# Optimization experiments

Hardware: AMD Instinct MI355X
Metric: run time of the kernel (lower is better)

The kernel has to match this reference:

```python
import jax, jax.numpy as jnp
import numpy as np
from jax.ops import segment_sum, segment_max

N, E, B = 100000, 400000, 2048
F_NODE, F_EDGE, G_DIM = 7, 3, 10
HID, H, C, L, T = 128, 4, 32, 4, 5
EPS = 1e-5
NEG_SLOPE = 0.2

def setup_inputs():
    key = jax.random.key(0)
    ks = iter(jax.random.split(key, 64))
    def nrm(shape, fan_in):
        return jax.random.normal(next(ks), shape, jnp.float32) / np.float32(np.sqrt(fan_in))
    return {
        "x": jax.random.normal(next(ks), (N, F_NODE), jnp.float32),
        "edge_index": jax.random.randint(next(ks), (2, E), 0, N),
        "edge_attr": jax.random.normal(next(ks), (E, F_EDGE), jnp.float32),
        "batch": jnp.sort(jax.random.randint(next(ks), (N,), 0, B)),
        "global_features": jax.random.normal(next(ks), (B, G_DIM), jnp.float32),
        "node_w": nrm((F_NODE, HID), F_NODE), "node_b": jnp.zeros((HID,), jnp.float32),
        "edge_w": nrm((F_EDGE, HID), F_EDGE), "edge_b": jnp.zeros((HID,), jnp.float32),
        "gat_lin_w": nrm((L, HID, H * C), HID),
        "gat_edge_w": nrm((L, HID, H * C), HID),
        "att_src": nrm((L, H, C), C), "att_dst": nrm((L, H, C), C), "att_edge": nrm((L, H, C), C),
        "gat_bias": jnp.zeros((L, H * C), jnp.float32),
        "bn_gamma": jnp.ones((L, HID), jnp.float32), "bn_beta": jnp.zeros((L, HID), jnp.float32),
        "bn_mean": jnp.zeros((L, HID), jnp.float32), "bn_var": jnp.ones((L, HID), jnp.float32),
        "gc_w": nrm((3 * HID, HID), 3 * HID), "gc_b": jnp.zeros((HID,), jnp.float32),
        "gf1_w": nrm((G_DIM, HID // 2), G_DIM), "gf1_b": jnp.zeros((HID // 2,), jnp.float32),
        "gf2_w": nrm((HID // 2, HID // 2), HID // 2), "gf2_b": jnp.zeros((HID // 2,), jnp.float32),
        "p1_w": nrm((HID + HID // 2, HID), HID + HID // 2), "p1_b": jnp.zeros((HID,), jnp.float32),
        "p2_w": nrm((HID, HID // 2), HID), "p2_b": jnp.zeros((HID // 2,), jnp.float32),
        "p3_w": nrm((HID // 2, T), HID // 2), "p3_b": jnp.zeros((T,), jnp.float32),
    }

def _forward(x, edge_attr, global_features,
             node_w, node_b, edge_w, edge_b,
             gat_lin_w, gat_edge_w, att_src, att_dst, att_edge, gat_bias,
             bn_gamma, bn_beta, bn_mean, bn_var,
             gc_w, gc_b, gf1_w, gf1_b, gf2_w, gf2_b,
             p1_w, p1_b, p2_w, p2_b, p3_w, p3_b,
             edge_index, batch):
    n = x.shape[0]
    b = global_features.shape[0]
    src, dst = edge_index[0], edge_index[1]
    loop = jnp.arange(n)

    h = x @ node_w + node_b                       # [N, HID]
    e = edge_attr @ edge_w + edge_b               # [E, HID]

    # PyG add_self_loops with fill_value='mean': self-loop edge feature is the
    # mean of incoming edge features (0 for isolated nodes).
    deg = segment_sum(jnp.ones((src.shape[0],), h.dtype), dst, num_segments=n)
    e_loop = segment_sum(e, dst, num_segments=n) / jnp.maximum(deg, 1.0)[:, None]
    fsrc = jnp.concatenate([src, loop])
    fdst = jnp.concatenate([dst, loop])
    fe = jnp.concatenate([e, e_loop], axis=0)     # [E+N, HID]

    for i in range(L):
        h_res = h
        xh = (h @ gat_lin_w[i]).reshape(n, H, C)
        eh = (fe @ gat_edge_w[i]).reshape(-1, H, C)
        a_s = jnp.einsum('nhc,hc->nh', xh, att_src[i])
        a_d = jnp.einsum('nhc,hc->nh', xh, att_dst[i])
        a_e = jnp.einsum('ehc,hc->eh', eh, att_edge[i])
        alpha = jax.nn.leaky_relu(a_s[fsrc] + a_d[fdst] + a_e, NEG_SLOPE)  # [E+N, H]
        # segment softmax over destination neighborhoods (self loops => nonempty)
        amax = segment_max(alpha, fdst, num_segments=n)
        expa = jnp.exp(alpha - amax[fdst])
        denom = segment_sum(expa, fdst, num_segments=n)
        coef = expa / denom[fdst]
        out = segment_sum(xh[fsrc] * coef[..., None], fdst, num_segments=n)
        out = out.reshape(n, H * C) + gat_bias[i]
        # BatchNorm (eval-mode running stats)
        out = (out - bn_mean[i]) * (bn_gamma[i] / jnp.sqrt(bn_var[i] + EPS)) + bn_beta[i]
        h = jax.nn.relu(out) + h_res

    # multi-pool readout
    cnt = segment_sum(jnp.ones((n,), h.dtype), batch, num_segments=b)
    gsum = segment_sum(h, batch, num_segments=b)
    gmean = gsum / jnp.maximum(cnt, 1.0)[:, None]
    gmax = segment_max(h, batch, num_segments=b)
    gmax = jnp.where(cnt[:, None] > 0, gmax, 0.0)
    graph = jnp.concatenate([gmean, gmax, gsum], axis=1)   # [B, 3*HID]
    graph = jax.nn.relu(graph @ gc_w + gc_b)
    glob = jax.nn.relu(global_features @ gf1_w + gf1_b) @ gf2_w + gf2_b
    comb = jnp.concatenate([graph, glob], axis=1)          # [B, HID + HID//2]
    hid = jax.nn.relu(comb @ p1_w + p1_b)
    hid = jax.nn.relu(hid @ p2_w + p2_b)
    return hid @ p3_w + p3_b                               # [B, T]

def reference(x, edge_index, edge_attr, batch, global_features,
              node_w, node_b, edge_w, edge_b,
              gat_lin_w, gat_edge_w, att_src, att_dst, att_edge, gat_bias,
              bn_gamma, bn_beta, bn_mean, bn_var,
              gc_w, gc_b, gf1_w, gf1_b, gf2_w, gf2_b,
              p1_w, p1_b, p2_w, p2_b, p3_w, p3_b):
    return _forward(x, edge_attr, global_features,
                    node_w, node_b, edge_w, edge_b,
                    gat_lin_w, gat_edge_w, att_src, att_dst, att_edge, gat_bias,
                    bn_gamma, bn_beta, bn_mean, bn_var,
                    gc_w, gc_b, gf1_w, gf1_b, gf2_w, gf2_b,
                    p1_w, p1_b, p2_w, p2_b, p3_w, p3_b,
                    edge_index, batch)
```

## Files before the change

### kernel.cpp

```cpp
#include <hip/hip_runtime.h>

#define N_NODES 100000
#define N_EDGES 400000
#define N_GRAPHS 2048
#define HID 128
#define NLAYER 4
#define TOUT 5
#define EPSV 1e-5f
#define SLOPE 0.2f
#define MAXDEG 32
#define NB 98
#define GEMM_BLOCKS 782

typedef float v4f __attribute__((ext_vector_type(4)));
typedef __bf16 v8bf __attribute__((ext_vector_type(8)));

static __device__ __forceinline__ unsigned short f2bf_bits(float f){
  unsigned u = __builtin_bit_cast(unsigned, f);
  unsigned r = u + 0x7fffu + ((u >> 16) & 1u);
  return (unsigned short)(r >> 16);
}
static __device__ __forceinline__ float bfbits2f(unsigned short s){
  unsigned u = ((unsigned)s) << 16;
  return __builtin_bit_cast(float, u);
}
static __device__ __forceinline__ float bflo(unsigned u){
  return __builtin_bit_cast(float, u << 16);
}
static __device__ __forceinline__ float bfhi(unsigned u){
  return __builtin_bit_cast(float, u & 0xffff0000u);
}
static __device__ __forceinline__ float lrelu(float v){
  return v>0.f ? v : SLOPE*v;
}


__global__ void k_setup(const float* __restrict__ gat_edge_w, const float* __restrict__ att_edge,
                        const float* __restrict__ edge_w, const float* __restrict__ edge_b,
                        const float* __restrict__ gat_bias, const float* __restrict__ gamma,
                        const float* __restrict__ beta, const float* __restrict__ mean,
                        const float* __restrict__ var, const float* __restrict__ gat_lin_w,
                        const float* __restrict__ att_src, const float* __restrict__ att_dst,
                        const float* __restrict__ x, const float* __restrict__ nw,
                        const float* __restrict__ nb, unsigned* __restrict__ h16,
                        float* __restrict__ mebuf, float* __restrict__ bnA, float* __restrict__ bnS,
                        unsigned short* __restrict__ whiE, unsigned short* __restrict__ wloE,
                        unsigned short* __restrict__ whi,
                        int* __restrict__ deg, int* __restrict__ fill){
  int bid = blockIdx.x, t = threadIdx.x;
  if(bid < 16){
    int wv = t>>6, lane = t&63;
    int o = bid*4 + wv;
    int li = (o<48)? (o&15) : (o-48);
    int f = o>>4;
    int l = li>>2, hh = li&3;
    int c = lane&31, kk = lane>>5;
    float at_c = att_edge[l*128 + hh*32 + c];
    float acc = 0.f;
    #pragma unroll 8
    for(int t2=0; t2<64; ++t2){
      int k = kk*64 + t2;
      float wk = (o<48)? edge_w[f*128+k] : edge_b[k];
      acc += wk * gat_edge_w[l*16384 + k*128 + hh*32 + c];
    }
    acc *= at_c;
    acc += __shfl_xor(acc,1); acc += __shfl_xor(acc,2); acc += __shfl_xor(acc,4);
    acc += __shfl_xor(acc,8); acc += __shfl_xor(acc,16); acc += __shfl_xor(acc,32);
    if(lane==0) mebuf[o] = acc;
  } else if(bid == 16){
    for(int i=t; i<NLAYER*HID; i+=256){
      int l_ = i>>7, pos = i&127, lane = pos>>2, j = pos&3;
      int ch = ((lane>>3)<<5) + ((lane&7)<<1) + ((j&1)<<4) + (j>>1);
      int src = l_*128 + ch;
      float A = gamma[src]*rsqrtf(var[src]+EPSV);
      bnA[i] = A;
      bnS[i] = (gat_bias[src]-mean[src])*A + beta[src];
    }
  } else if(bid <= 1040){
    int wave = t>>6, lane = t&63;
    int i = (bid-17)*8 + wave*2 + (lane>>5);
    int l_ = i>>11, rest = i&2047, kp = rest>>4, col = rest&15;
    int sub = lane&31;
    float val = 0.f;
    if(col < 8){
      int h_ = col&3, isdst = col>>2;
      int ch = ((kp>>5)<<5) + ((kp&1)<<4) + ((kp&31)>>1);
      const float* at = (isdst? att_dst : att_src);
      val = gat_lin_w[l_*16384 + ch*128 + h_*32 + sub] * at[l_*128 + h_*32 + sub];
    }
    val += __shfl_xor(val,1); val += __shfl_xor(val,2); val += __shfl_xor(val,4);
    val += __shfl_xor(val,8); val += __shfl_xor(val,16);
    if(sub == 0){
      unsigned short hi = f2bf_bits(val);
      unsigned short lo = f2bf_bits(val - bfbits2f(hi));
      int kb=kp>>5, quad=(kp>>3)&3, jj=kp&7, lane2=quad*16+col;
      int dst = ((l_*4+kb)*64 + lane2)*8 + jj;
      whiE[dst]=hi; wloE[dst]=lo;
    }
  } else if(bid <= 1296){
    int tg = (bid-1041)*256 + t;
    int base = tg>>9, off = tg&511;
    int l = base>>5, kb=(base>>3)&3, cg=base&7;
    int lane = off>>3, j = off&7;
    int quad = lane>>4, r = lane&15;
    int kp = kb*32 + quad*8 + j;
    int k = ((kp>>5)<<5) | ((kp&1)<<4) | ((kp&31)>>1);
    whi[tg] = f2bf_bits(gat_lin_w[l*16384 + k*128 + cg*16 + r]);
  } else if(bid <= 1687){
    int tg = (bid-1297)*256 + t;
    if(tg < N_NODES){ deg[tg]=0; fill[tg]=0; }
  } else {
    int node = (bid-1688)*4 + (t>>6);
    int c = t&63;
    int ch = ((c>>4)<<5) + (c&15);
    float a0 = nb[ch], a1 = nb[ch+16];
    #pragma unroll
    for(int f=0; f<7; ++f){
      float xv = x[node*7+f];
      a0 += xv*nw[f*HID+ch];
      a1 += xv*nw[f*HID+ch+16];
    }
    unsigned p = (unsigned)f2bf_bits(a0) | ((unsigned)f2bf_bits(a1)<<16);
    h16[(size_t)node*64 + c] = p;
  }
}

__global__ void k_deg(const int* __restrict__ ei, int* __restrict__ deg){
  int e = blockIdx.x*256 + threadIdx.x;
  if(e < N_EDGES) atomicAdd(&deg[ei[N_EDGES+e]], 1);
}

__global__ void k_scan1(const int* __restrict__ deg, int* __restrict__ part){
  __shared__ int s[256];
  int t=threadIdx.x; int base = blockIdx.x*1024 + t*4;
  int sum=0;
  #pragma unroll
  for(int j=0;j<4;++j){ int i=base+j; sum += (i<N_NODES)? deg[i]:0; }
  s[t]=sum; __syncthreads();
  for(int off=128; off>0; off>>=1){ if(t<off) s[t]+=s[t+off]; __syncthreads(); }
  if(t==0) part[blockIdx.x]=s[0];
}
__global__ void k_scan3(const int* __restrict__ deg, const int* __restrict__ part,
                        int* __restrict__ rowptr){
  __shared__ int s[256];
  int t=threadIdx.x, b=blockIdx.x;
  int g = 0, tot = 0;
  for(int i=0;i<NB;++i){ int v = part[i]; g += (i<b)? v : 0; tot += v; }
  if(b==0 && t==0) rowptr[N_NODES]=tot;
  int base = b*1024 + t*4;
  int v[4]; int sum=0; int pre[4];
  #pragma unroll
  for(int j=0;j<4;++j){ int i=base+j; v[j]=(i<N_NODES)?deg[i]:0; pre[j]=sum; sum+=v[j]; }
  s[t]=sum; __syncthreads();
  for(int off=1; off<256; off<<=1){
    int xv = (t>=off)? s[t-off]:0; __syncthreads();
    s[t]+=xv; __syncthreads();
  }
  int toff = (t>0)? s[t-1]:0;
  #pragma unroll
  for(int j=0;j<4;++j){ int i=base+j; if(i<N_NODES) rowptr[i]=g+toff+pre[j]; }
}

__global__ void k_gemm(const unsigned short* __restrict__ h16,
                       const unsigned short* __restrict__ whi,
                       const unsigned short* __restrict__ whiE,
                       const unsigned short* __restrict__ wloE,
                       unsigned* __restrict__ xhb, float* __restrict__ as_, float* __restrict__ ad_,
                       const int* __restrict__ ei, const float* __restrict__ ea,
                       const int* __restrict__ rowptr, int* __restrict__ fill,
                       int* __restrict__ csr_src, float* __restrict__ ea_csr){
  if(blockIdx.x >= GEMM_BLOCKS){
    int e = (blockIdx.x - GEMM_BLOCKS)*256 + threadIdx.x;
    if(e < N_EDGES){
      int dst = ei[N_EDGES+e];
      int pos = rowptr[dst] + atomicAdd(&fill[dst],1);
      csr_src[pos] = ei[e];
      v4f q = {ea[e*3], ea[e*3+1], ea[e*3+2], 0.f};
      ((v4f*)ea_csr)[pos] = q;
    }
    return;
  }
  __shared__ unsigned sxh[4][2][16*68];
  int wave = threadIdx.x>>6, lane = threadIdx.x&63;
  int base = blockIdx.x*128;
  int q = lane>>4, r = lane&15;
  int r0[2];
  r0[0] = base + wave*16;
  r0[1] = base + 64 + wave*16;
  if(r0[0] > N_NODES-16) r0[0] = N_NODES-16;
  if(r0[1] > N_NODES-16) r0[1] = N_NODES-16;
  v8bf av[2][4];
  #pragma unroll
  for(int tt=0;tt<2;++tt){
    const unsigned short* hrow = h16 + (size_t)(r0[tt] + r)*HID;
    #pragma unroll
    for(int kb=0;kb<4;++kb)
      av[tt][kb] = *(const v8bf*)(hrow + kb*32 + q*8);
  }
  v4f acc[2][8];
  #pragma unroll
  for(int cg=0;cg<8;++cg){
    v4f a0 = {0.f,0.f,0.f,0.f}, a1 = {0.f,0.f,0.f,0.f};
    #pragma unroll
    for(int kb=0;kb<4;++kb){
      v8bf bhi = *(const v8bf*)(whi + ((kb*8+cg)*64 + lane)*8);
      a0 = __builtin_amdgcn_mfma_f32_16x16x32_bf16(av[0][kb], bhi, a0, 0,0,0);
      a1 = __builtin_amdgcn_mfma_f32_16x16x32_bf16(av[1][kb], bhi, a1, 0,0,0);
    }
    acc[0][cg]=a0; acc[1][cg]=a1;
  }
  v4f acc8[2] = {{0.f,0.f,0.f,0.f},{0.f,0.f,0.f,0.f}};
  #pragma unroll
  for(int kb=0;kb<4;++kb){
    v8bf bhi = *(const v8bf*)(whiE + (kb*64 + lane)*8);
    v8bf blo = *(const v8bf*)(wloE + (kb*64 + lane)*8);
    #pragma unroll
    for(int tt=0;tt<2;++tt){
      acc8[tt] = __builtin_amdgcn_mfma_f32_16x16x32_bf16(av[tt][kb], blo, acc8[tt], 0,0,0);
      acc8[tt] = __builtin_amdgcn_mfma_f32_16x16x32_bf16(av[tt][kb], bhi, acc8[tt], 0,0,0);
    }
  }
  #pragma unroll
  for(int tt=0;tt<2;++tt){
    #pragma unroll
    for(int m=0;m<4;++m){
      #pragma unroll
      for(int reg=0;reg<4;++reg){
        unsigned pack = (unsigned)f2bf_bits(acc[tt][2*m][reg]) | ((unsigned)f2bf_bits(acc[tt][2*m+1][reg])<<16);
        sxh[wave][tt][(q*4+reg)*68 + m*16 + r] = pack;
      }
    }
  }
  __syncthreads();
  {
    int rr = lane>>4, c4 = lane&15;
    #pragma unroll
    for(int tt=0;tt<2;++tt){
      #pragma unroll
      for(int rg=0; rg<4; ++rg){
        int i = rg*4 + rr;
        uint4 v = *(const uint4*)&sxh[wave][tt][i*68 + c4*4];
        *(uint4*)(xhb + (size_t)(r0[tt] + i)*64 + c4*4) = v;
      }
    }
  }
  #pragma unroll
  for(int tt=0;tt<2;++tt){
    if(r < 4){
      #pragma unroll
      for(int reg=0;reg<4;++reg)
        as_[(size_t)(r0[tt] + q*4 + reg)*4 + r] = acc8[tt][reg];
    } else if(r < 8){
      #pragma unroll
      for(int reg=0;reg<4;++reg)
        ad_[(size_t)(r0[tt] + q*4 + reg)*4 + (r-4)] = acc8[tt][reg];
    }
  }
}

__global__ void k_aggr(const unsigned* __restrict__ xhb, const float* __restrict__ as_,
    const float* __restrict__ ad_, const float* __restrict__ ea_csr,
    const float* __restrict__ mebuf,
    const int* __restrict__ rowptr, const int* __restrict__ csr_src,
    const float* __restrict__ bnA_l, const float* __restrict__ bnS_l,
    unsigned* __restrict__ h16, int layer){
  __shared__ float lds_coef[4][MAXDEG*4];
  __shared__ int   lds_src[4][MAXDEG];
  int w = threadIdx.x>>6, lane = threadIdx.x&63;
  int node = blockIdx.x*4 + w;
  if(node >= N_NODES) return;
  int s = rowptr[node], e = rowptr[node+1];
  int deg = e - s;
  int l = lane&31, half = lane>>5, hh2 = l>>3;
  const uint2* xrow = (const uint2*)xhb;
  float a0,a1,a2,a3;

  if(deg <= MAXDEG){
    int eidx = lane>>2, h = lane&3;
    int li = layer*4+h;
    float mec0=mebuf[li], mec1=mebuf[16+li], mec2=mebuf[32+li], meb=mebuf[48+li];
    float ad_h = ad_[node*4+h];
    int j0 = eidx;
    float t0 = 0.f, g0 = 0.f;
    int s0 = node;
    bool v0 = (j0 < deg);
    if(v0){
      s0 = csr_src[s+j0];
      v4f qq = ((const v4f*)ea_csr)[s+j0];
      t0 = qq.x*mec0 + qq.y*mec1 + qq.z*mec2;
      g0 = lrelu(as_[s0*4+h] + ad_h + t0 + meb);
    }
    float ts, ds, inv;
    if(deg <= 16){
      ts = t0;
      ts += __shfl_xor(ts,4); ts += __shfl_xor(ts,8);
      ts += __shfl_xor(ts,16); ts += __shfl_xor(ts,32);
      float lt = (deg>0) ? ts/(float)deg + meb : 0.f;
      float al = lrelu(as_[node*4+h] + ad_h + lt);
      float e0 = v0 ? __expf(g0-al) : 0.f;
      ds = e0;
      ds += __shfl_xor(ds,4); ds += __shfl_xor(ds,8);
      ds += __shfl_xor(ds,16); ds += __shfl_xor(ds,32);
      inv = 1.f/(ds+1.f);
      lds_src[w][j0] = s0;
      lds_coef[w][j0*4+h] = e0*inv;
    } else {
      int j1 = 16+eidx;
      float t1 = 0.f, g1 = 0.f;
      int s1 = node;
      bool v1 = (j1 < deg);
      if(v1){
        s1 = csr_src[s+j1];
        v4f qq = ((const v4f*)ea_csr)[s+j1];
        t1 = qq.x*mec0 + qq.y*mec1 + qq.z*mec2;
        g1 = lrelu(as_[s1*4+h] + ad_h + t1 + meb);
      }
      ts = t0+t1;
      ts += __shfl_xor(ts,4); ts += __shfl_xor(ts,8);
      ts += __shfl_xor(ts,16); ts += __shfl_xor(ts,32);
      float lt = ts/(float)deg + meb;
      float al = lrelu(as_[node*4+h] + ad_h + lt);
      float e0 = v0 ? __expf(g0-al) : 0.f;
      float e1 = v1 ? __expf(g1-al) : 0.f;
      ds = e0+e1;
      ds += __shfl_xor(ds,4); ds += __shfl_xor(ds,8);
      ds += __shfl_xor(ds,16); ds += __shfl_xor(ds,32);
      inv = 1.f/(ds+1.f);
      if(h==0){ lds_src[w][j0]=s0; lds_src[w][j1]=s1; }
      lds_coef[w][j0*4+h] = e0*inv;
      lds_coef[w][j1*4+h] = e1*inv;
    }
    float cs4 = __shfl(inv, hh2);
    uint2 su = xrow[(size_t)node*32 + l];
    int pdeg = (deg+3)&~3;
    a0=a1=a2=a3=0.f;
    for(int j=0;j<pdeg;j+=4){
      float ca = lds_coef[w][(j+half)*4+hh2];
      float cb = lds_coef[w][(j+2+half)*4+hh2];
      int sa = lds_src[w][j+half], sb = lds_src[w][j+2+half];
      uint2 ua = xrow[(size_t)sa*32+l];
      uint2 ub = xrow[(size_t)sb*32+l];
      a0 += ca*bflo(ua.x) + cb*bflo(ub.x);
      a1 += ca*bfhi(ua.x) + cb*bfhi(ub.x);
      a2 += ca*bflo(ua.y) + cb*bflo(ub.y);
      a3 += ca*bfhi(ua.y) + cb*bfhi(ub.y);
    }
    a0 += __shfl_xor(a0,32); a1 += __shfl_xor(a1,32);
    a2 += __shfl_xor(a2,32); a3 += __shfl_xor(a3,32);
    a0 += cs4*bflo(su.x); a1 += cs4*bfhi(su.x);
    a2 += cs4*bflo(su.y); a3 += cs4*bfhi(su.y);
  } else {
    int li = layer*4+hh2;
    float mec0=mebuf[li], mec1=mebuf[16+li], mec2=mebuf[32+li], meb=mebuf[48+li];
    float adv = ad_[node*4+hh2];
    float ts = 0.f;
    for(int j=s;j<e;++j){
      v4f qq = ((const v4f*)ea_csr)[j];
      ts += qq.x*mec0 + qq.y*mec1 + qq.z*mec2;
    }
    float al = lrelu(as_[node*4+hh2] + adv + ts/(float)deg + meb);
    float m = al, d = 1.f;
    uint2 su = xrow[(size_t)node*32 + l];
    float c0=bflo(su.x),c1=bfhi(su.x),c2=bflo(su.y),c3=bfhi(su.y);
    for(int j=s;j<e;++j){
      int sr = csr_src[j];
      v4f qq = ((const v4f*)ea_csr)[j];
      float b = lrelu(as_[sr*4+hh2] + adv + qq.x*mec0+qq.y*mec1+qq.z*mec2+meb);
      uint2 uv = xrow[(size_t)sr*32 + l];
      float nm = fmaxf(m,b);
      float sc = __expf(m-nm), eb = __expf(b-nm);
      d = d*sc + eb;
      c0 = c0*sc + eb*bflo(uv.x); c1 = c1*sc + eb*bfhi(uv.x);
      c2 = c2*sc + eb*bflo(uv.y); c3 = c3*sc + eb*bfhi(uv.y);
      m = nm;
    }
    float inv2 = 1.f/d;
    a0=c0*inv2; a1=c1*inv2; a2=c2*inv2; a3=c3*inv2;
  }

  if(half==0){
    const v4f* A4 = (const v4f*)bnA_l;
    const v4f* S4 = (const v4f*)bnS_l;
    v4f A = A4[l], S = S4[l];
    uint2 hr = ((const uint2*)h16)[(size_t)node*32 + l];
    float o0 = fmaxf(a0*A.x+S.x, 0.f) + bflo(hr.x);
    float o1 = fmaxf(a1*A.y+S.y, 0.f) + bfhi(hr.x);
    float o2 = fmaxf(a2*A.z+S.z, 0.f) + bflo(hr.y);
    float o3 = fmaxf(a3*A.w+S.w, 0.f) + bfhi(hr.y);
    uint2 p;
    p.x = (unsigned)f2bf_bits(o0) | ((unsigned)f2bf_bits(o1)<<16);
    p.y = (unsigned)f2bf_bits(o2) | ((unsigned)f2bf_bits(o3)<<16);
    ((uint2*)h16)[(size_t)node*32 + l] = p;
  }
}

__global__ void k_tail(const unsigned* __restrict__ h16, const int* __restrict__ batch,
   const float* __restrict__ gf,
   const float* __restrict__ gc_w, const float* __restrict__ gc_b,
   const float* __restrict__ gf1_w, const float* __restrict__ gf1_b,
   const float* __restrict__ gf2_w, const float* __restrict__ gf2_b,
   const float* __restrict__ p1_w, const float* __restrict__ p1_b,
   const float* __restrict__ p2_w, const float* __restrict__ p2_b,
   const float* __restrict__ p3_w, const float* __restrict__ p3_b,
   float* __restrict__ out){
  __shared__ float sg[384];
  __shared__ int sb[2];
  __shared__ float comb[192];
  __shared__ float hid1[64];
  __shared__ float r1[128];
  __shared__ float r2[64];
  int g = blockIdx.x, t = threadIdx.x;
  if(t < 2){
    int target = g + t;
    int lo=0, hi=N_NODES;
    while(lo<hi){ int mid=(lo+hi)>>1; if(batch[mid] < target) lo=mid+1; else hi=mid; }
    sb[t]=lo;
  }
  __syncthreads();
  {
    int s = sb[0], e = sb[1];
    int u = ((t>>5)<<4) + (t&15);
    int hiflag = (t>>4)&1;
    float sum=0.f, mx=-3.4e38f;
    for(int i=s;i<e;++i){
      unsigned uv = h16[(size_t)i*64 + u];
      float v = hiflag ? bfhi(uv) : bflo(uv);
      sum+=v; mx=fmaxf(mx,v);
    }
    int cnt = e-s;
    float meanv = sum / (float)(cnt>1?cnt:1);
    if(cnt==0) mx=0.f;
    sg[t] = meanv;
    sg[128+t] = mx;
    sg[256+t] = sum;
  }
  if(t<64){
    float a = gf1_b[t];
    #pragma unroll
    for(int i=0;i<10;++i) a += gf[g*10+i]*gf1_w[i*64+t];
    hid1[t] = fmaxf(a,0.f);
  }
  __syncthreads();
  if(t<64){
    float a = gf2_b[t];
    for(int k=0;k<64;++k) a += hid1[k]*gf2_w[k*64+t];
    comb[128+t] = a;
  }
  {
    float a = gc_b[t];
    for(int k=0;k<384;++k) a += sg[k]*gc_w[k*128+t];
    comb[t] = fmaxf(a,0.f);
  }
  __syncthreads();
  {
    float a = p1_b[t];
    for(int k=0;k<192;++k) a += comb[k]*p1_w[k*128+t];
    r1[t] = fmaxf(a,0.f);
  }
  __syncthreads();
  if(t<64){
    float a = p2_b[t];
    for(int k=0;k<128;++k) a += r1[k]*p2_w[k*64+t];
    r2[t] = fmaxf(a,0.f);
  }
  __syncthreads();
  if(t<TOUT){
    float a = p3_b[t];
    for(int k=0;k<64;++k) a += r2[k]*p3_w[k*TOUT+t];
    out[g*TOUT+t] = a;
  }
}

extern "C" void kernel_launch(void* const* d_in, const int* in_sizes, int n_in,
                              void* d_out, int out_size, void* d_ws, size_t ws_size,
                              hipStream_t stream){
  (void)in_sizes; (void)n_in; (void)out_size; (void)ws_size;
  const float* x        = (const float*)d_in[0];
  const int*   ei       = (const int*)d_in[1];
  const float* ea       = (const float*)d_in[2];
  const int*   batch    = (const int*)d_in[3];
  const float* gfin     = (const float*)d_in[4];
  const float* node_w   = (const float*)d_in[5];
  const float* node_b   = (const float*)d_in[6];
  const float* edge_w   = (const float*)d_in[7];
  const float* edge_b   = (const float*)d_in[8];
  const float* gat_lin_w  = (const float*)d_in[9];
  const float* gat_edge_w = (const float*)d_in[10];
  const float* att_src  = (const float*)d_in[11];
  const float* att_dst  = (const float*)d_in[12];
  const float* att_edge = (const float*)d_in[13];
  const float* gat_bias = (const float*)d_in[14];
  const float* bn_gamma = (const float*)d_in[15];
  const float* bn_beta  = (const float*)d_in[16];
  const float* bn_mean  = (const float*)d_in[17];
  const float* bn_var   = (const float*)d_in[18];
  const float* gc_w = (const float*)d_in[19];
  const float* gc_b = (const float*)d_in[20];
  const float* gf1_w = (const float*)d_in[21];
  const float* gf1_b = (const float*)d_in[22];
  const float* gf2_w = (const float*)d_in[23];
  const float* gf2_b = (const float*)d_in[24];
  const float* p1_w = (const float*)d_in[25];
  const float* p1_b = (const float*)d_in[26];
  const float* p2_w = (const float*)d_in[27];
  const float* p2_b = (const float*)d_in[28];
  const float* p3_w = (const float*)d_in[29];
  const float* p3_b = (const float*)d_in[30];
  float* out = (float*)d_out;

  char* w = (char*)d_ws;
  size_t o = 0;
  auto carve = [&](size_t bytes)->char*{
    char* p = w + o; o += (bytes + 255) & ~(size_t)255; return p;
  };
  unsigned* xhb = (unsigned*)carve((size_t)N_NODES*64*4);
  unsigned* h16 = (unsigned*)carve((size_t)N_NODES*64*4);
  float* ea_csr = (float*)carve((size_t)N_EDGES*4*4);
  float* as_    = (float*)carve((size_t)N_NODES*4*4);
  float* ad_    = (float*)carve((size_t)N_NODES*4*4);
  int* deg      = (int*)carve((size_t)N_NODES*4);
  int* rowptr   = (int*)carve((size_t)(N_NODES+1)*4);
  int* fill     = (int*)carve((size_t)N_NODES*4);
  int* csr_src  = (int*)carve((size_t)N_EDGES*4);
  int* part     = (int*)carve(1024*4);
  float* mebuf  = (float*)carve(64*4);
  float* bnA    = (float*)carve((size_t)NLAYER*HID*4);
  float* bnS    = (float*)carve((size_t)NLAYER*HID*4);
  unsigned short* whi = (unsigned short*)carve(65536*2);
  unsigned short* whiE = (unsigned short*)carve(8192*2);
  unsigned short* wloE = (unsigned short*)carve(8192*2);

  k_setup<<<1688 + N_NODES/4, 256, 0, stream>>>(gat_edge_w, att_edge, edge_w, edge_b,
        gat_bias, bn_gamma, bn_beta, bn_mean, bn_var,
        gat_lin_w, att_src, att_dst, x, node_w, node_b, h16,
        mebuf, bnA, bnS, whiE, wloE, whi, deg, fill);
  k_deg<<<(N_EDGES+255)/256, 256, 0, stream>>>(ei, deg);
  k_scan1<<<NB,256,0,stream>>>(deg, part);
  k_scan3<<<NB,256,0,stream>>>(deg, part, rowptr);

  for(int l=0;l<NLAYER;++l){
    int gb = (l==0) ? GEMM_BLOCKS + (N_EDGES+255)/256 : GEMM_BLOCKS;
    k_gemm<<<gb,256,0,stream>>>((const unsigned short*)h16,
        whi + l*16384, whiE + l*2048, wloE + l*2048,
        xhb, as_, ad_, ei, ea, rowptr, fill, csr_src, ea_csr);
    k_aggr<<<(N_NODES+3)/4,256,0,stream>>>(xhb, as_, ad_, ea_csr, mebuf,
        rowptr, csr_src, bnA + l*128, bnS + l*128, h16, l);
  }

  k_tail<<<N_GRAPHS,128,0,stream>>>(h16, batch, gfin, gc_w, gc_b, gf1_w, gf1_b,
        gf2_w, gf2_b, p1_w, p1_b, p2_w, p2_b, p3_w, p3_b, out);
}
```

Measured before the change: 491.0 us.

## Map one node per half-wavefront in GAT aggregation kernel

The aggregation kernel now assigns each node to 32 lanes instead of a full 64-lane wavefront, so each block handles eight nodes and the grid shrinks by half. The fast path now covers degree ≤16 (two edge slots per lane group), and the neighbor gather loop steps two edges at a time. The cross-half reduction and the half-idle epilogue go away. The aim is to cut idle lanes and wavefront count for the low average degree. The cost is that nodes with degree 17–32 now fall into the serial online-softmax path, and the two halves of a wave can diverge.

```diff
diff --git a/kernel.cpp b/kernel.cpp
--- a/kernel.cpp
+++ b/kernel.cpp
@@ -8,7 +8,6 @@
 #define TOUT 5
 #define EPSV 1e-5f
 #define SLOPE 0.2f
-#define MAXDEG 32
 #define NB 98
 #define GEMM_BLOCKS 782
 
@@ -264,19 +263,20 @@
     const int* __restrict__ rowptr, const int* __restrict__ csr_src,
     const float* __restrict__ bnA_l, const float* __restrict__ bnS_l,
     unsigned* __restrict__ h16, int layer){
-  __shared__ float lds_coef[4][MAXDEG*4];
-  __shared__ int   lds_src[4][MAXDEG];
-  int w = threadIdx.x>>6, lane = threadIdx.x&63;
-  int node = blockIdx.x*4 + w;
+  __shared__ float lds_coef[8][16*4];
+  __shared__ int   lds_src[8][16];
+  int hw = threadIdx.x>>5, lh = threadIdx.x&31;
+  int lane = threadIdx.x&63;
+  int node = blockIdx.x*8 + hw;
   if(node >= N_NODES) return;
   int s = rowptr[node], e = rowptr[node+1];
   int deg = e - s;
-  int l = lane&31, half = lane>>5, hh2 = l>>3;
+  int hh2 = lh>>3;
   const uint2* xrow = (const uint2*)xhb;
   float a0,a1,a2,a3;
 
-  if(deg <= MAXDEG){
-    int eidx = lane>>2, h = lane&3;
+  if(deg <= 16){
+    int eidx = lh>>2, h = lh&3;
     int li = layer*4+h;
     float mec0=mebuf[li], mec1=mebuf[16+li], mec2=mebuf[32+li], meb=mebuf[48+li];
     float ad_h = ad_[node*4+h];
@@ -291,21 +291,19 @@
       g0 = lrelu(as_[s0*4+h] + ad_h + t0 + meb);
     }
     float ts, ds, inv;
-    if(deg <= 16){
+    if(deg <= 8){
       ts = t0;
-      ts += __shfl_xor(ts,4); ts += __shfl_xor(ts,8);
-      ts += __shfl_xor(ts,16); ts += __shfl_xor(ts,32);
+      ts += __shfl_xor(ts,4); ts += __shfl_xor(ts,8); ts += __shfl_xor(ts,16);
       float lt = (deg>0) ? ts/(float)deg + meb : 0.f;
       float al = lrelu(as_[node*4+h] + ad_h + lt);
       float e0 = v0 ? __expf(g0-al) : 0.f;
       ds = e0;
-      ds += __shfl_xor(ds,4); ds += __shfl_xor(ds,8);
-      ds += __shfl_xor(ds,16); ds += __shfl_xor(ds,32);
+      ds += __shfl_xor(ds,4); ds += __shfl_xor(ds,8); ds += __shfl_xor(ds,16);
       inv = 1.f/(ds+1.f);
-      lds_src[w][j0] = s0;
-      lds_coef[w][j0*4+h] = e0*inv;
+      if(h==0) lds_src[hw][j0] = s0;
+      lds_coef[hw][j0*4+h] = e0*inv;
     } else {
-      int j1 = 16+eidx;
+      int j1 = 8+eidx;
       float t1 = 0.f, g1 = 0.f;
       int s1 = node;
       bool v1 = (j1 < deg);
@@ -316,37 +314,33 @@
         g1 = lrelu(as_[s1*4+h] + ad_h + t1 + meb);
       }
       ts = t0+t1;
-      ts += __shfl_xor(ts,4); ts += __shfl_xor(ts,8);
-      ts += __shfl_xor(ts,16); ts += __shfl_xor(ts,32);
+      ts += __shfl_xor(ts,4); ts += __shfl_xor(ts,8); ts += __shfl_xor(ts,16);
       float lt = ts/(float)deg + meb;
       float al = lrelu(as_[node*4+h] + ad_h + lt);
       float e0 = v0 ? __expf(g0-al) : 0.f;
       float e1 = v1 ? __expf(g1-al) : 0.f;
       ds = e0+e1;
-      ds += __shfl_xor(ds,4); ds += __shfl_xor(ds,8);
-      ds += __shfl_xor(ds,16); ds += __shfl_xor(ds,32);
+      ds += __shfl_xor(ds,4); ds += __shfl_xor(ds,8); ds += __shfl_xor(ds,16);
       inv = 1.f/(ds+1.f);
-      if(h==0){ lds_src[w][j0]=s0; lds_src[w][j1]=s1; }
-      lds_coef[w][j0*4+h] = e0*inv;
-      lds_coef[w][j1*4+h] = e1*inv;
-    }
-    float cs4 = __shfl(inv, hh2);
-    uint2 su = xrow[(size_t)node*32 + l];
-    int pdeg = (deg+3)&~3;
+      if(h==0){ lds_src[hw][j0]=s0; lds_src[hw][j1]=s1; }
+      lds_coef[hw][j0*4+h] = e0*inv;
+      lds_coef[hw][j1*4+h] = e1*inv;
+    }
+    float cs4 = __shfl(inv, (lane&32) | hh2);
+    uint2 su = xrow[(size_t)node*32 + lh];
+    int pdeg = (deg+1)&~1;
     a0=a1=a2=a3=0.f;
-    for(int j=0;j<pdeg;j+=4){
-      float ca = lds_coef[w][(j+half)*4+hh2];
-      float cb = lds_coef[w][(j+2+half)*4+hh2];
-      int sa = lds_src[w][j+half], sb = lds_src[w][j+2+half];
-      uint2 ua = xrow[(size_t)sa*32+l];
-      uint2 ub = xrow[(size_t)sb*32+l];
+    for(int j=0;j<pdeg;j+=2){
+      float ca = lds_coef[hw][j*4+hh2];
+      float cb = lds_coef[hw][(j+1)*4+hh2];
+      int sa = lds_src[hw][j], sb = lds_src[hw][j+1];
+      uint2 ua = xrow[(size_t)sa*32+lh];
+      uint2 ub = xrow[(size_t)sb*32+lh];
       a0 += ca*bflo(ua.x) + cb*bflo(ub.x);
       a1 += ca*bfhi(ua.x) + cb*bfhi(ub.x);
       a2 += ca*bflo(ua.y) + cb*bflo(ub.y);
       a3 += ca*bfhi(ua.y) + cb*bfhi(ub.y);
     }
-    a0 += __shfl_xor(a0,32); a1 += __shfl_xor(a1,32);
-    a2 += __shfl_xor(a2,32); a3 += __shfl_xor(a3,32);
     a0 += cs4*bflo(su.x); a1 += cs4*bfhi(su.x);
     a2 += cs4*bflo(su.y); a3 += cs4*bfhi(su.y);
   } else {
@@ -360,13 +354,13 @@
     }
     float al = lrelu(as_[node*4+hh2] + adv + ts/(float)deg + meb);
     float m = al, d = 1.f;
-    uint2 su = xrow[(size_t)node*32 + l];
+    uint2 su = xrow[(size_t)node*32 + lh];
     float c0=bflo(su.x),c1=bfhi(su.x),c2=bflo(su.y),c3=bfhi(su.y);
     for(int j=s;j<e;++j){
       int sr = csr_src[j];
       v4f qq = ((const v4f*)ea_csr)[j];
       float b = lrelu(as_[sr*4+hh2] + adv + qq.x*mec0+qq.y*mec1+qq.z*mec2+meb);
-      uint2 uv = xrow[(size_t)sr*32 + l];
+      uint2 uv = xrow[(size_t)sr*32 + lh];
       float nm = fmaxf(m,b);
       float sc = __expf(m-nm), eb = __expf(b-nm);
       d = d*sc + eb;
@@ -378,11 +372,11 @@
     a0=c0*inv2; a1=c1*inv2; a2=c2*inv2; a3=c3*inv2;
   }
 
-  if(half==0){
+  {
     const v4f* A4 = (const v4f*)bnA_l;
     const v4f* S4 = (const v4f*)bnS_l;
-    v4f A = A4[l], S = S4[l];
-    uint2 hr = ((const uint2*)h16)[(size_t)node*32 + l];
+    v4f A = A4[lh], S = S4[lh];
+    uint2 hr = ((const uint2*)h16)[(size_t)node*32 + lh];
     float o0 = fmaxf(a0*A.x+S.x, 0.f) + bflo(hr.x);
     float o1 = fmaxf(a1*A.y+S.y, 0.f) + bfhi(hr.x);
     float o2 = fmaxf(a2*A.z+S.z, 0.f) + bflo(hr.y);
@@ -390,7 +384,7 @@
     uint2 p;
     p.x = (unsigned)f2bf_bits(o0) | ((unsigned)f2bf_bits(o1)<<16);
     p.y = (unsigned)f2bf_bits(o2) | ((unsigned)f2bf_bits(o3)<<16);
-    ((uint2*)h16)[(size_t)node*32 + l] = p;
+    ((uint2*)h16)[(size_t)node*32 + lh] = p;
   }
 }
 
@@ -543,7 +537,7 @@
     k_gemm<<<gb,256,0,stream>>>((const unsigned short*)h16,
         whi + l*16384, whiE + l*2048, wloE + l*2048,
         xhb, as_, ad_, ei, ea, rowptr, fill, csr_src, ea_csr);
-    k_aggr<<<(N_NODES+3)/4,256,0,stream>>>(xhb, as_, ad_, ea_csr, mebuf,
+    k_aggr<<<(N_NODES+7)/8,256,0,stream>>>(xhb, as_, ad_, ea_csr, mebuf,
         rowptr, csr_src, bnA + l*128, bnS + l*128, h16, l);
   }
 
```

Result: faster. 437.8 us (-10.8%).
